# Optimization experiments

Hardware: AMD Instinct MI355X
Metric: run time of the kernel (lower is better)

Reference implementation:

```python
import jax, jax.numpy as jnp
import numpy as np

_LOG2PI = float(np.log(2.0 * np.pi))


def setup_inputs() -> dict:
    key = jax.random.key(0)
    ks = jax.random.split(key, 9)
    B, T, S, A, O = 64, 128, 512, 16, 4096
    regime = jax.random.randint(ks[0], (B,), 0, 2).astype(jnp.float32)
    obs = jax.random.randint(ks[1], (T + 1, B), 0, O, dtype=jnp.int32)
    rewards = jax.random.normal(ks[2], (T + 1, B), jnp.float32)
    dones = jnp.zeros((T + 1, B), jnp.float32)
    actions = jax.random.randint(ks[3], (T, B), 0, A, dtype=jnp.int32)
    prior_logits = jax.random.normal(ks[4], (S,), jnp.float32)
    trans_logits = jax.random.normal(ks[5], (A, S, S), jnp.float32)
    obs_logits = jax.random.normal(ks[6], (S, O), jnp.float32)
    policy_logits = jax.random.normal(ks[7], (S, A), jnp.float32)
    r_mu = jax.random.normal(ks[8], (S,), jnp.float32)
    r_logsig = jnp.zeros((S,), jnp.float32)
    return {"regime": regime, "obs": obs, "rewards": rewards, "dones": dones,
            "actions": actions, "prior_logits": prior_logits,
            "trans_logits": trans_logits, "obs_logits": obs_logits,
            "policy_logits": policy_logits, "r_mu": r_mu, "r_logsig": r_logsig}


def _log_prob(regime, obs, rewards, dones, actions, prior_logits, trans_logits,
              obs_logits, policy_logits, r_mu, r_logsig):
    # normalized log-prob tables (tabular instantiation of AugmentedModel)
    log_prior = jax.nn.log_softmax(prior_logits)              # [S]
    log_trans = jax.nn.log_softmax(trans_logits, axis=-1)     # [A,S,S]
    log_obs = jax.nn.log_softmax(obs_logits, axis=-1)         # [S,O]
    log_pol = jax.nn.log_softmax(policy_logits, axis=-1)      # [S,A]
    lse = jax.scipy.special.logsumexp

    def emis(o, r):  # log q(o|s) + log q(r|s) -> [B,S]
        lo = log_obs.T[o]                                      # [B,S] gather
        lr = (-0.5 * (((r[:, None] - r_mu[None, :]) * jnp.exp(-r_logsig)[None, :]) ** 2)
              - r_logsig[None, :] - 0.5 * _LOG2PI)             # [B,S]
        return lo + lr

    def act_term(a, done):  # masked log q(a|s) -> [B,S]
        la = log_pol.T[a]                                      # [B,S]
        la = jnp.where((done == 1.0)[:, None], jnp.zeros_like(la), la)
        la = jnp.where((regime == 1.0)[:, None], jnp.zeros_like(la), la)
        return la

    T = actions.shape[0]
    B = regime.shape[0]

    # t = 0
    was_done = jnp.zeros((B,), rewards.dtype)
    done0 = dones[0]
    lq_sorda = log_prior[None, :] + emis(obs[0], rewards[0]) + act_term(actions[0], done0)
    lq_orda = lse(lq_sorda, axis=-1) * (1.0 - was_done)        # [B]
    log_prob = lq_orda
    lq_s_h = lq_sorda - lq_orda[:, None]
    # belief propagation through transition: [B,S,1] + [B,S,S] -> lse over prev state
    lq_snext_h = lse(lq_s_h[:, :, None] + log_trans[actions[0]], axis=1)

    def step(carry, xs):  # t = 1 .. T-1 (has an action)
        log_prob, was_done, lq_s_hprev = carry
        o, r, d, a = xs
        done = jnp.maximum(was_done, d)
        lq = lq_s_hprev + emis(o, r) + act_term(a, done)
        lq_orda = lse(lq, axis=-1) * (1.0 - was_done)
        log_prob = jnp.where(jnp.isinf(log_prob), log_prob, log_prob + lq_orda)
        lq_s_h = lq - lq_orda[:, None]
        lq_snext = lse(lq_s_h[:, :, None] + log_trans[a], axis=1)
        return (log_prob, done, lq_snext), None

    xs = (obs[1:T], rewards[1:T], dones[1:T], actions[1:T])
    (log_prob, was_done, lq_s_hprev), _ = jax.lax.scan(
        step, (log_prob, done0, lq_snext_h), xs)

    # final step t = T (no action term)
    lq = lq_s_hprev + emis(obs[T], rewards[T])
    lq_ord = lse(lq, axis=-1) * (1.0 - was_done)
    log_prob = jnp.where(jnp.isinf(log_prob), log_prob, log_prob + lq_ord)
    return log_prob


def reference(regime, obs, rewards, dones, actions, prior_logits, trans_logits,
              obs_logits, policy_logits, r_mu, r_logsig):
    return _log_prob(regime, obs, rewards, dones, actions, prior_logits,
                     trans_logits, obs_logits, policy_logits, r_mu, r_logsig)
```

## Files before the change

kernel.cpp:

```cpp
#include <hip/hip_runtime.h>
#include <math.h>

#define DI __device__ __forceinline__

constexpr int BB = 64;
constexpr int TT = 128;
constexpr int SS = 512;
constexpr int AA = 16;
constexpr int OO = 4096;
constexpr float LOG2PI = 1.8378770664093453f;
constexpr float LOG4096 = 8.317766166719343f;

typedef float f32x4 __attribute__((ext_vector_type(4)));

DI void lds_barrier() {
    asm volatile("s_waitcnt lgkmcnt(0)\n\ts_barrier" ::: "memory");
}

typedef __attribute__((address_space(3))) unsigned int as3_u32;
typedef __attribute__((address_space(1))) const unsigned int as1_u32;
DI void dma1k(const unsigned char* g, unsigned char* l) {
    __builtin_amdgcn_global_load_lds((as1_u32*)g, (as3_u32*)l, 16, 0, 0);
}

DI unsigned int f32_to_e4m3(float x) {
    unsigned int u = __float_as_uint(x);
    unsigned int lsb = (u >> 20) & 1u;
    unsigned int rounded = u + 0x7ffffu + lsb;
    int e8 = (int)(rounded >> 23) - 120;
    unsigned int m3 = (rounded >> 20) & 7u;
    unsigned int norm = ((unsigned int)e8 << 3) | m3;
    int sub = __float2int_rn(x * 512.0f);
    return (e8 <= 0) ? (unsigned int)sub : norm;
}

DI float bflyMax(float v) {
#pragma unroll
    for (int off = 32; off; off >>= 1) v = fmaxf(v, __shfl_xor(v, off));
    return v;
}
DI float bflySum(float v) {
#pragma unroll
    for (int off = 32; off; off >>= 1) v += __shfl_xor(v, off);
    return v;
}
DI float halfMax(float v) {
#pragma unroll
    for (int off = 16; off; off >>= 1) v = fmaxf(v, __shfl_xor(v, off));
    return v;
}
DI float halfSum(float v) {
#pragma unroll
    for (int off = 16; off; off >>= 1) v += __shfl_xor(v, off);
    return v;
}

template <int NW>
DI float blockMax(float v, float* wr) {
    v = bflyMax(v);
    const int lane = threadIdx.x & 63, wv = threadIdx.x >> 6;
    if (lane == 0) wr[wv] = v;
    __syncthreads();
    float r = wr[0];
#pragma unroll
    for (int i = 1; i < NW; ++i) r = fmaxf(r, wr[i]);
    __syncthreads();
    return r;
}
template <int NW>
DI float blockSum(float v, float* wr) {
    v = bflySum(v);
    const int lane = threadIdx.x & 63, wv = threadIdx.x >> 6;
    if (lane == 0) wr[wv] = v;
    __syncthreads();
    float r = wr[0];
#pragma unroll
    for (int i = 1; i < NW; ++i) r += wr[i];
    __syncthreads();
    return r;
}


__global__ __launch_bounds__(1024) void k_pack(const float* __restrict__ tl,
                                               unsigned char* __restrict__ PB) {
    __shared__ unsigned char lds[16384];
    const int a = blockIdx.x >> 4;
    const int kt = blockIdx.x & 15;
    const int tid = threadIdx.x;
    const int r = tid >> 5;
    const int nt = tid & 31;
    const int k = kt * 32 + r;
    const float* row = tl + ((size_t)a * SS + k) * SS + nt * 16;

    float x[16];
#pragma unroll
    for (int i = 0; i < 4; ++i) {
        float4 v = ((const float4*)row)[i];
        x[4 * i] = v.x; x[4 * i + 1] = v.y; x[4 * i + 2] = v.z; x[4 * i + 3] = v.w;
    }
    float mx = -INFINITY;
#pragma unroll
    for (int i = 0; i < 16; ++i) mx = fmaxf(mx, x[i]);
    mx = halfMax(mx);
    float e[16];
    float sm = 0.f;
#pragma unroll
    for (int i = 0; i < 16; ++i) { e[i] = __expf(x[i] - mx); sm += e[i]; }
    sm = halfSum(sm);
    const float scale = 256.0f / sm;

    const int base = (nt >> 1) * 1024 + ((r >> 3) * 16) * 16 + (nt & 1) * 8 + (r & 7);
#pragma unroll
    for (int i = 0; i < 16; ++i) {
        lds[base + i * 16] = (unsigned char)f32_to_e4m3(e[i] * scale);
    }
    __syncthreads();

    ulonglong2* dst = (ulonglong2*)(PB + (size_t)(a * 16 + kt) * 16384);
    dst[tid] = ((const ulonglong2*)lds)[tid];
}

__global__ __launch_bounds__(256) void k_obs_stats(const float* __restrict__ ol,
                                                   float* __restrict__ mo,
                                                   float* __restrict__ lo) {
    __shared__ float wr[4];
    const int s = blockIdx.x;
    const float* in = ol + (size_t)s * OO;
    const int tid = threadIdx.x;
    float mx = -INFINITY;
    for (int i = tid; i < OO; i += 256) mx = fmaxf(mx, in[i]);
    float m = blockMax<4>(mx, wr);
    float sm = 0.f;
    for (int i = tid; i < OO; i += 256) sm += __expf(in[i] - m);
    float sum = blockSum<4>(sm, wr);
    if (tid == 0) { mo[s] = m; lo[s] = __logf(sum); }
}

__global__ __launch_bounds__(256) void k_obsT(const float* __restrict__ ol,
                                              const float* __restrict__ mo,
                                              const float* __restrict__ lo,
                                              float* __restrict__ obsT) {
    __shared__ float tile[64][65];
    const int tO = blockIdx.x % (OO / 64);
    const int tS = blockIdx.x / (OO / 64);
    const int o0 = tO * 64, s0 = tS * 64;
    const int cc = threadIdx.x & 63, rr = threadIdx.x >> 6;
#pragma unroll
    for (int j = 0; j < 16; ++j) {
        int r = rr + j * 4;
        tile[r][cc] = ol[(size_t)(s0 + r) * OO + o0 + cc] - mo[s0 + r] - lo[s0 + r];
    }
    __syncthreads();
#pragma unroll
    for (int j = 0; j < 16; ++j) {
        int r = rr + j * 4;
        obsT[(size_t)(o0 + r) * SS + s0 + cc] = tile[cc][r];
    }
}

__global__ __launch_bounds__(512) void k_main(
    const float* __restrict__ regime, const int* __restrict__ obs,
    const float* __restrict__ rewards, const float* __restrict__ dones,
    const int* __restrict__ actions, const float* __restrict__ prior_logits,
    const unsigned char* __restrict__ PB, const float* __restrict__ obsT,
    const float* __restrict__ policy_logits, const float* __restrict__ r_mu,
    const float* __restrict__ r_logsig, float* __restrict__ out) {
    __shared__ unsigned char stage[3 * 16384];
    __shared__ float wrm[8], wrs[8];
    __shared__ unsigned char p8[4 * 144 + 16];
    __shared__ float lqprev[SS];
    __shared__ int obs_l[TT + 1];
    __shared__ float rew_l[TT + 1];
    __shared__ float done_l[TT + 1];
    __shared__ int act_l[TT];

    const int b = blockIdx.x;
    const int tid = threadIdx.x;
    const int wv = tid >> 6, lane = tid & 63, quad = lane >> 4;
    const int s = tid;

    if (tid <= TT) {
        obs_l[tid] = obs[tid * BB + b];
        rew_l[tid] = rewards[tid * BB + b];
        done_l[tid] = dones[tid * BB + b];
        if (tid < TT) act_l[tid] = actions[tid * BB + b];
    }
    float la16[16];
    {
        const float4* pr4 = (const float4*)(policy_logits + (size_t)s * AA);
        float4 v0 = pr4[0], v1 = pr4[1], v2 = pr4[2], v3 = pr4[3];
        la16[0] = v0.x; la16[1] = v0.y; la16[2] = v0.z; la16[3] = v0.w;
        la16[4] = v1.x; la16[5] = v1.y; la16[6] = v1.z; la16[7] = v1.w;
        la16[8] = v2.x; la16[9] = v2.y; la16[10] = v2.z; la16[11] = v2.w;
        la16[12] = v3.x; la16[13] = v3.y; la16[14] = v3.z; la16[15] = v3.w;
        float mx = la16[0];
#pragma unroll
        for (int i = 1; i < 16; ++i) mx = fmaxf(mx, la16[i]);
        float sm = 0.f;
#pragma unroll
        for (int i = 0; i < 16; ++i) sm += __expf(la16[i] - mx);
        float ls = mx + __logf(sm);
#pragma unroll
        for (int i = 0; i < 16; ++i) la16[i] -= ls;
    }
    const float rm = r_mu[s];
    const float rls = r_logsig[s];
    const float inv_sig = __expf(-rls);
    const float reg = regime[b];

    float px = prior_logits[s];
    {
        float wm0 = bflyMax(px);
        if (lane == 0) wrm[wv] = wm0;
    }
    lds_barrier();
    float pm = wrm[0];
#pragma unroll
    for (int i = 1; i < 8; ++i) pm = fmaxf(pm, wrm[i]);
    {
        float ws0 = bflySum(__expf(px - pm));
        if (lane == 0) wrs[wv] = ws0;
    }
    lds_barrier();
    float psum = wrs[0];
#pragma unroll
    for (int i = 1; i < 8; ++i) psum += wrs[i];
    const float prior_reg = px - pm - __logf(psum);

    float obsv = obsT[(size_t)obs_l[0] * SS + s];

    float log_prob = 0.f;
    float was_done = 0.f;

    for (int t = 0; t < TT; ++t) {
        const float r = rew_l[t];
        const int a = __builtin_amdgcn_readfirstlane(act_l[t]);
        const float d = done_l[t];
        const float done = fmaxf(was_done, d);

        const unsigned char* PBa = PB + (size_t)a * (16 * 16384);
        unsigned char* mystage = stage + wv * 2048;

#pragma unroll
        for (int c = 0; c < 3; ++c) {
            const unsigned char* g = PBa + c * 16384 + (2 * wv) * 1024 + lane * 16;
            unsigned char* l = mystage + c * 16384;
            dma1k(g, l);
            dma1k(g + 1024, l + 1024);
        }
        asm volatile("" ::: "memory");
        float obsv_next = obsT[(size_t)obs_l[t + 1] * SS + s];
        asm volatile("" ::: "memory");

        float diff = (r - rm) * inv_sig;
        float emis = obsv - 0.5f * diff * diff - rls - 0.5f * LOG2PI;
        float base_in = (t == 0) ? prior_reg : lqprev[s];
        float la = la16[0];
#pragma unroll
        for (int i = 1; i < 16; ++i) la = (a == i) ? la16[i] : la;
        if (done == 1.0f || reg == 1.0f) la = 0.f;
        float lq = base_in + emis + la;

        float wmax = bflyMax(lq);
        if (lane == 0) wrm[wv] = wmax;
        lds_barrier();
        float m = wrm[0];
#pragma unroll
        for (int i = 1; i < 8; ++i) m = fmaxf(m, wrm[i]);

        float exv = __expf(lq - m);
        p8[((s >> 3) & 3) * 144 + (s >> 5) * 8 + (s & 7)] =
            (unsigned char)f32_to_e4m3(exv * 16.0f);
        float wsum = bflySum(exv);
        if (lane == 0) wrs[wv] = wsum;
        lds_barrier();
        float sum = wrs[0];
#pragma unroll
        for (int i = 1; i < 8; ++i) sum += wrs[i];
        float lse = m + __logf(sum);
        float lq_orda = lse * (1.0f - was_done);
        if (!isinf(log_prob)) log_prob += lq_orda;
        was_done = done;

        const float basev = m - lq_orda - LOG4096;
        f32x4 acc0 = {0.f, 0.f, 0.f, 0.f};
        f32x4 acc1 = {0.f, 0.f, 0.f, 0.f};
        f32x4 acc2 = {0.f, 0.f, 0.f, 0.f};
        f32x4 acc3 = {0.f, 0.f, 0.f, 0.f};

#define CHUNK(c, WN)                                                            \
        {                                                                       \
            asm volatile("s_waitcnt vmcnt(" #WN ")" ::: "memory");              \
            const unsigned char* sb = mystage + ((c) % 3) * 16384 + lane * 16;  \
            ulonglong2 f0 = *(const ulonglong2*)(sb);                           \
            ulonglong2 f1 = *(const ulonglong2*)(sb + 1024);                    \
            long af = *(const long long*)(p8 + quad * 144 + (c) * 8);           \
            acc0 = __builtin_amdgcn_mfma_f32_16x16x32_fp8_fp8((long)f0.x, af, acc0, 0, 0, 0); \
            acc1 = __builtin_amdgcn_mfma_f32_16x16x32_fp8_fp8((long)f0.y, af, acc1, 0, 0, 0); \
            acc2 = __builtin_amdgcn_mfma_f32_16x16x32_fp8_fp8((long)f1.x, af, acc2, 0, 0, 0); \
            acc3 = __builtin_amdgcn_mfma_f32_16x16x32_fp8_fp8((long)f1.y, af, acc3, 0, 0, 0); \
            if ((c) + 3 < 16) {                                                 \
                asm volatile("s_waitcnt lgkmcnt(0)" ::: "memory");              \
                const unsigned char* g = PBa + ((c) + 3) * 16384 + (2 * wv) * 1024 + lane * 16; \
                unsigned char* l = mystage + ((c) % 3) * 16384;                 \
                dma1k(g, l);                                                    \
                dma1k(g + 1024, l + 1024);                                      \
            }                                                                   \
        }
        CHUNK(0, 5)  CHUNK(1, 5)  CHUNK(2, 5)  CHUNK(3, 4)
        CHUNK(4, 4)  CHUNK(5, 4)  CHUNK(6, 4)  CHUNK(7, 4)
        CHUNK(8, 4)  CHUNK(9, 4)  CHUNK(10, 4) CHUNK(11, 4)
        CHUNK(12, 4) CHUNK(13, 4) CHUNK(14, 2) CHUNK(15, 0)
#undef CHUNK

        if (lane < 16) {
            lqprev[wv * 64 + lane]      = basev + __logf(acc0[0]);
            lqprev[wv * 64 + 16 + lane] = basev + __logf(acc1[0]);
            lqprev[wv * 64 + 32 + lane] = basev + __logf(acc2[0]);
            lqprev[wv * 64 + 48 + lane] = basev + __logf(acc3[0]);
        }
        lds_barrier();
        obsv = obsv_next;
    }

    {
        const float r = rew_l[TT];
        float diff = (r - rm) * inv_sig;
        float emis = obsv - 0.5f * diff * diff - rls - 0.5f * LOG2PI;
        float lq = lqprev[s] + emis;
        float wmax = bflyMax(lq);
        if (lane == 0) wrm[wv] = wmax;
        lds_barrier();
        float m = wrm[0];
#pragma unroll
        for (int i = 1; i < 8; ++i) m = fmaxf(m, wrm[i]);
        float wsum = bflySum(__expf(lq - m));
        if (lane == 0) wrs[wv] = wsum;
        lds_barrier();
        float sum = wrs[0];
#pragma unroll
        for (int i = 1; i < 8; ++i) sum += wrs[i];
        float lse = m + __logf(sum);
        float lq_ord = lse * (1.0f - was_done);
        if (!isinf(log_prob)) log_prob += lq_ord;
    }

    if (tid == 0) out[b] = log_prob;
}

extern "C" void kernel_launch(void* const* d_in, const int* in_sizes, int n_in,
                              void* d_out, int out_size, void* d_ws, size_t ws_size,
                              hipStream_t stream) {
    const float* regime = (const float*)d_in[0];
    const int* obs = (const int*)d_in[1];
    const float* rewards = (const float*)d_in[2];
    const float* dones = (const float*)d_in[3];
    const int* actions = (const int*)d_in[4];
    const float* prior_logits = (const float*)d_in[5];
    const float* trans_logits = (const float*)d_in[6];
    const float* obs_logits = (const float*)d_in[7];
    const float* policy_logits = (const float*)d_in[8];
    const float* r_mu = (const float*)d_in[9];
    const float* r_logsig = (const float*)d_in[10];
    float* out = (float*)d_out;

    char* ws = (char*)d_ws;
    unsigned char* PB = (unsigned char*)ws;
    float* obsT = (float*)(ws + (size_t)AA * SS * SS);
    float* mo = (float*)(ws + (size_t)AA * SS * SS + (size_t)OO * SS * 4);
    float* lo = mo + SS;

    k_pack<<<256, 1024, 0, stream>>>(trans_logits, PB);
    k_obs_stats<<<SS, 256, 0, stream>>>(obs_logits, mo, lo);
    k_obsT<<<(OO / 64) * (SS / 64), 256, 0, stream>>>(obs_logits, mo, lo, obsT);
    k_main<<<BB, 512, 0, stream>>>(regime, obs, rewards, dones, actions, prior_logits,
                                   PB, obsT, policy_logits, r_mu, r_logsig, out);
}
```

Measured before the change: 539.2 us.

## Deepen LDS staging to 8 chunks and software-pipeline LDS reads with MFMA

Enlarges the per-step LDS staging ring for the fp8 transition block from 3 to 8 chunks, so more global-to-LDS DMA loads are in flight at the start of each time step. The MFMA loop is restructured so the LDS read of chunk k+1 overlaps the MFMA of chunk k, with explicit vmcnt/lgkmcnt waits. The A-fragments (p8) are preloaded into registers, and the obs gather is issued before the DMAs. This uses 128KB of LDS plus more registers, which limits the block to one per CU. The vmcnt accounting also has to count the obs load correctly.

```diff
diff --git a/kernel.cpp b/kernel.cpp
--- a/kernel.cpp
+++ b/kernel.cpp
@@ -165,7 +165,7 @@
     const unsigned char* __restrict__ PB, const float* __restrict__ obsT,
     const float* __restrict__ policy_logits, const float* __restrict__ r_mu,
     const float* __restrict__ r_logsig, float* __restrict__ out) {
-    __shared__ unsigned char stage[3 * 16384];
+    __shared__ unsigned char stage[8 * 16384];
     __shared__ float wrm[8], wrs[8];
     __shared__ unsigned char p8[4 * 144 + 16];
     __shared__ float lqprev[SS];
@@ -239,17 +239,17 @@
         const float done = fmaxf(was_done, d);
 
         const unsigned char* PBa = PB + (size_t)a * (16 * 16384);
-        unsigned char* mystage = stage + wv * 2048;
-
-#pragma unroll
-        for (int c = 0; c < 3; ++c) {
+        unsigned char* ms = stage + wv * 2048;
+
+        float obsv_next = obsT[(size_t)obs_l[t + 1] * SS + s];
+        asm volatile("" ::: "memory");
+#pragma unroll
+        for (int c = 0; c < 8; ++c) {
             const unsigned char* g = PBa + c * 16384 + (2 * wv) * 1024 + lane * 16;
-            unsigned char* l = mystage + c * 16384;
+            unsigned char* l = ms + c * 16384;
             dma1k(g, l);
             dma1k(g + 1024, l + 1024);
         }
-        asm volatile("" ::: "memory");
-        float obsv_next = obsT[(size_t)obs_l[t + 1] * SS + s];
         asm volatile("" ::: "memory");
 
         float diff = (r - rm) * inv_sig;
@@ -283,35 +283,62 @@
         was_done = done;
 
         const float basev = m - lq_orda - LOG4096;
+        long afr[16];
+#pragma unroll
+        for (int kt = 0; kt < 16; ++kt)
+            afr[kt] = *(const long long*)(p8 + quad * 144 + kt * 8);
+
         f32x4 acc0 = {0.f, 0.f, 0.f, 0.f};
         f32x4 acc1 = {0.f, 0.f, 0.f, 0.f};
         f32x4 acc2 = {0.f, 0.f, 0.f, 0.f};
         f32x4 acc3 = {0.f, 0.f, 0.f, 0.f};
-
-#define CHUNK(c, WN)                                                            \
-        {                                                                       \
-            asm volatile("s_waitcnt vmcnt(" #WN ")" ::: "memory");              \
-            const unsigned char* sb = mystage + ((c) % 3) * 16384 + lane * 16;  \
-            ulonglong2 f0 = *(const ulonglong2*)(sb);                           \
-            ulonglong2 f1 = *(const ulonglong2*)(sb + 1024);                    \
-            long af = *(const long long*)(p8 + quad * 144 + (c) * 8);           \
-            acc0 = __builtin_amdgcn_mfma_f32_16x16x32_fp8_fp8((long)f0.x, af, acc0, 0, 0, 0); \
-            acc1 = __builtin_amdgcn_mfma_f32_16x16x32_fp8_fp8((long)f0.y, af, acc1, 0, 0, 0); \
-            acc2 = __builtin_amdgcn_mfma_f32_16x16x32_fp8_fp8((long)f1.x, af, acc2, 0, 0, 0); \
-            acc3 = __builtin_amdgcn_mfma_f32_16x16x32_fp8_fp8((long)f1.y, af, acc3, 0, 0, 0); \
-            if ((c) + 3 < 16) {                                                 \
-                asm volatile("s_waitcnt lgkmcnt(0)" ::: "memory");              \
-                const unsigned char* g = PBa + ((c) + 3) * 16384 + (2 * wv) * 1024 + lane * 16; \
-                unsigned char* l = mystage + ((c) % 3) * 16384;                 \
-                dma1k(g, l);                                                    \
-                dma1k(g + 1024, l + 1024);                                      \
-            }                                                                   \
+        ulonglong2 fa0, fa1, fb0, fb1;
+
+#define WAITV(n) asm volatile("s_waitcnt vmcnt(" #n ")" ::: "memory")
+#define WAITL(n) asm volatile("s_waitcnt lgkmcnt(" #n ")" ::: "memory")
+#define DSRD(kt, F0, F1)                                                       \
+        {                                                                      \
+            const unsigned char* sb = ms + ((kt) & 7) * 16384 + lane * 16;     \
+            F0 = *(const ulonglong2*)sb;                                       \
+            F1 = *(const ulonglong2*)(sb + 1024);                              \
         }
-        CHUNK(0, 5)  CHUNK(1, 5)  CHUNK(2, 5)  CHUNK(3, 4)
-        CHUNK(4, 4)  CHUNK(5, 4)  CHUNK(6, 4)  CHUNK(7, 4)
-        CHUNK(8, 4)  CHUNK(9, 4)  CHUNK(10, 4) CHUNK(11, 4)
-        CHUNK(12, 4) CHUNK(13, 4) CHUNK(14, 2) CHUNK(15, 0)
-#undef CHUNK
+#define MF(kt, F0, F1)                                                         \
+        {                                                                      \
+            long af = afr[kt];                                                 \
+            acc0 = __builtin_amdgcn_mfma_f32_16x16x32_fp8_fp8((long)F0.x, af, acc0, 0, 0, 0); \
+            acc1 = __builtin_amdgcn_mfma_f32_16x16x32_fp8_fp8((long)F0.y, af, acc1, 0, 0, 0); \
+            acc2 = __builtin_amdgcn_mfma_f32_16x16x32_fp8_fp8((long)F1.x, af, acc2, 0, 0, 0); \
+            acc3 = __builtin_amdgcn_mfma_f32_16x16x32_fp8_fp8((long)F1.y, af, acc3, 0, 0, 0); \
+        }
+#define DMA(kt)                                                                \
+        {                                                                      \
+            const unsigned char* g = PBa + (kt) * 16384 + (2 * wv) * 1024 + lane * 16; \
+            unsigned char* l = ms + ((kt) & 7) * 16384;                        \
+            dma1k(g, l);                                                       \
+            dma1k(g + 1024, l + 1024);                                         \
+        }
+        WAITV(14); DSRD(0, fa0, fa1);
+        WAITV(12); DSRD(1, fb0, fb1);  WAITL(2); MF(0, fa0, fa1);  DMA(8);
+        WAITV(12); DSRD(2, fa0, fa1);  WAITL(2); MF(1, fb0, fb1);  DMA(9);
+        WAITV(12); DSRD(3, fb0, fb1);  WAITL(2); MF(2, fa0, fa1);  DMA(10);
+        WAITV(12); DSRD(4, fa0, fa1);  WAITL(2); MF(3, fb0, fb1);  DMA(11);
+        WAITV(12); DSRD(5, fb0, fb1);  WAITL(2); MF(4, fa0, fa1);  DMA(12);
+        WAITV(12); DSRD(6, fa0, fa1);  WAITL(2); MF(5, fb0, fb1);  DMA(13);
+        WAITV(12); DSRD(7, fb0, fb1);  WAITL(2); MF(6, fa0, fa1);  DMA(14);
+        WAITV(12); DSRD(8, fa0, fa1);  WAITL(2); MF(7, fb0, fb1);  DMA(15);
+        WAITV(12); DSRD(9, fb0, fb1);  WAITL(2); MF(8, fa0, fa1);
+        WAITV(10); DSRD(10, fa0, fa1); WAITL(2); MF(9, fb0, fb1);
+        WAITV(8);  DSRD(11, fb0, fb1); WAITL(2); MF(10, fa0, fa1);
+        WAITV(6);  DSRD(12, fa0, fa1); WAITL(2); MF(11, fb0, fb1);
+        WAITV(4);  DSRD(13, fb0, fb1); WAITL(2); MF(12, fa0, fa1);
+        WAITV(2);  DSRD(14, fa0, fa1); WAITL(2); MF(13, fb0, fb1);
+        WAITV(0);  DSRD(15, fb0, fb1); WAITL(2); MF(14, fa0, fa1);
+        WAITL(0);  MF(15, fb0, fb1);
+#undef WAITV
+#undef WAITL
+#undef DSRD
+#undef MF
+#undef DMA
 
         if (lane < 16) {
             lqprev[wv * 64 + lane]      = basev + __logf(acc0[0]);
```

Result: slower. 578.1 us (+7.2%).
